# Kernel tuning notes

Measured on AMD Instinct MI355X. Metric: run time of the kernel, lower is better.

## Reference

```python
import jax, jax.numpy as jnp
import numpy as np

VOCAB, EMBED, HIDDEN = 50000, 300, 1024
BATCH, SEQ = 64, 128


def _lstm_params(key, in_dim, hid):
    k = 1.0 / np.sqrt(hid)
    k1, k2, k3, k4 = jax.random.split(key, 4)
    return (
        jax.random.uniform(k1, (4 * hid, in_dim), jnp.float32, -k, k),  # W_ih
        jax.random.uniform(k2, (4 * hid, hid), jnp.float32, -k, k),     # W_hh
        jax.random.uniform(k3, (4 * hid,), jnp.float32, -k, k),          # b_ih
        jax.random.uniform(k4, (4 * hid,), jnp.float32, -k, k),          # b_hh
    )


def setup_inputs() -> dict:
    key = jax.random.key(0)
    ke, kf, kb, ki = jax.random.split(key, 4)
    embed_table = jax.random.normal(ke, (VOCAB, EMBED), jnp.float32)
    Wih_f, Whh_f, bih_f, bhh_f = _lstm_params(kf, EMBED, HIDDEN)
    Wih_b, Whh_b, bih_b, bhh_b = _lstm_params(kb, EMBED, HIDDEN)
    inputs = jax.random.randint(ki, (BATCH, SEQ), 0, VOCAB, jnp.int64 if jax.config.jax_enable_x64 else jnp.int32)
    return {
        "embed_table": embed_table,
        "Wih_f": Wih_f, "Whh_f": Whh_f, "bih_f": bih_f, "bhh_f": bhh_f,
        "Wih_b": Wih_b, "Whh_b": Whh_b, "bih_b": bih_b, "bhh_b": bhh_b,
        "inputs": inputs,
    }


def _lstm_cell(x, h, c, Wih, Whh, bih, bhh):
    # torch.nn.LSTMCell gate layout: i, f, g, o
    gates = x @ Wih.T + h @ Whh.T + (bih + bhh)
    i, f, g, o = jnp.split(gates, 4, axis=-1)
    i, f, o = jax.nn.sigmoid(i), jax.nn.sigmoid(f), jax.nn.sigmoid(o)
    g = jnp.tanh(g)
    c_new = f * c + i * g
    h_new = o * jnp.tanh(c_new)
    return h_new, c_new


def reference(embed_table, Wih_f, Whh_f, bih_f, bhh_f, Wih_b, Whh_b, bih_b, bhh_b, inputs):
    embeds = embed_table[inputs]  # [B, T, E]
    B = inputs.shape[0]
    zeros = jnp.zeros((B, HIDDEN), embeds.dtype)
    # Faithful to the original bug: the forward loop always uses the all-zero
    # (never-updated) backward state and overwrites h each step, so the result
    # equals a single LSTMCell step on the LAST token with zero (h, c).
    h_fwd, _ = _lstm_cell(embeds[:, -1], zeros, zeros, Wih_f, Whh_f, bih_f, bhh_f)
    # Backward loop: h carries over, but c stays zero forever (bug preserved).
    xs = jnp.flip(embeds, axis=1).transpose(1, 0, 2)  # time-major, reversed: [T, B, E]

    def step(h, x):
        h_new, _ = _lstm_cell(x, h, zeros, Wih_b, Whh_b, bih_b, bhh_b)
        return h_new, None

    h_bwd, _ = jax.lax.scan(step, zeros, xs)
    return jnp.concatenate((h_fwd, h_bwd), axis=1)  # [B, 2*HIDDEN]
```

## Files before the change

### kernel.cpp

```cpp
#include <hip/hip_runtime.h>
#include <stdint.h>

static constexpr int BB = 64;
static constexpr int TT = 128;
static constexpr int EE = 300;
static constexpr int HH = 1024;
static constexpr int OUTW = 2 * HH;
static constexpr int NB  = 256;
static constexpr int NT  = 512;


typedef __attribute__((ext_vector_type(8))) short bf16x8;
typedef __attribute__((ext_vector_type(4))) float f32x4;
union U16 { uint4 u; bf16x8 v; };

__device__ __forceinline__ unsigned short f2bf(float f) {
  uint32_t u = __float_as_uint(f);
  uint32_t r = (u + 0x7fffu + ((u >> 16) & 1u)) >> 16;
  return (unsigned short)r;
}
__device__ __forceinline__ float bf2f(unsigned short h) {
  return __uint_as_float(((uint32_t)h) << 16);
}

__device__ __forceinline__ void gload16_sc(uint4& d, const void* p) {
  asm volatile("global_load_dwordx4 %0, %1, off sc0 sc1" : "=v"(d) : "v"(p));
}
__device__ __forceinline__ void gload16_nc(uint4& d, const void* p) {
  asm volatile("global_load_dwordx4 %0, %1, off" : "=v"(d) : "v"(p));
}

__global__ __launch_bounds__(256) void k_stage(const float* __restrict__ tbl,
                                               const int* __restrict__ inp,
                                               unsigned char* __restrict__ xfrag,
                                               float* __restrict__ xT0) {
  __shared__ float tile[EE * 65];
  __shared__ int toks[BB];
  const int s = blockIdx.x;
  const int tid = threadIdx.x;
  if (tid < BB) toks[tid] = inp[tid * TT + (TT - 1 - s)];
  __syncthreads();
  for (int f = tid; f < BB * EE; f += 256) {
    int b = f / EE, e = f - b * EE;
    tile[e * 65 + b] = tbl[(size_t)toks[b] * EE + e];
  }
  __syncthreads();
  if (s == 0) {
    for (int f = tid; f < EE * BB; f += 256) {
      int e = f >> 6, b = f & 63;
      xT0[f] = tile[e * 65 + b];
    }
  }
  const int ksub = tid & 3, col = (tid >> 2) & 63;
  unsigned char* base = xfrag + (size_t)s * 98304;
  for (int kb = 0; kb < 12; ++kb) {
    uint32_t hi[4], lo[4];
#pragma unroll
    for (int j2 = 0; j2 < 4; ++j2) {
      int e0 = kb * 32 + ksub * 8 + 2 * j2;
      float f0 = (e0     < EE) ? tile[e0 * 65 + col]      : 0.f;
      float f1 = (e0 + 1 < EE) ? tile[(e0 + 1) * 65 + col] : 0.f;
      unsigned short h0 = f2bf(f0), h1 = f2bf(f1);
      unsigned short l0 = f2bf(f0 - bf2f(h0)), l1 = f2bf(f1 - bf2f(h1));
      hi[j2] = (uint32_t)h0 | ((uint32_t)h1 << 16);
      lo[j2] = (uint32_t)l0 | ((uint32_t)l1 << 16);
    }
    unsigned char* p = base + kb * 8192 + col * 128 + ksub * 16;
    *(uint4*)p        = make_uint4(hi[0], hi[1], hi[2], hi[3]);
    *(uint4*)(p + 64) = make_uint4(lo[0], lo[1], lo[2], lo[3]);
  }
}

__global__ __launch_bounds__(256) void k_fwd(const float* __restrict__ Wih,
                                             const float* __restrict__ bih,
                                             const float* __restrict__ bhh,
                                             const float* __restrict__ xT,
                                             float* __restrict__ out) {
  const int g = blockIdx.x * 256 + threadIdx.x;
  const int j = g >> 6, b = g & 63;
  const float* wi = Wih + (size_t)j * EE;
  const float* wg = Wih + (size_t)(2 * HH + j) * EE;
  const float* wo = Wih + (size_t)(3 * HH + j) * EE;
  float si = 0.f, sg = 0.f, so = 0.f;
  for (int e = 0; e < EE; ++e) {
    float x = xT[e * 64 + b];
    si += x * wi[e];
    sg += x * wg[e];
    so += x * wo[e];
  }
  si += bih[j] + bhh[j];
  sg += bih[2 * HH + j] + bhh[2 * HH + j];
  so += bih[3 * HH + j] + bhh[3 * HH + j];
  float iv = 1.f / (1.f + expf(-si));
  float gv = tanhf(sg);
  float ov = 1.f / (1.f + expf(-so));
  out[b * OUTW + j] = ov * tanhf(iv * gv);
}

__global__ __launch_bounds__(NT, 2) void k_rec(const float* __restrict__ Whh,
                                               const float* __restrict__ Wih,
                                               const float* __restrict__ bih,
                                               const float* __restrict__ bhh,
                                               const unsigned char* __restrict__ xfrag,
                                               unsigned char* __restrict__ h0ex,
                                               unsigned char* __restrict__ h1ex,
                                               unsigned int* __restrict__ syncc,
                                               float* __restrict__ out) {
  __shared__ float red[4 * 4 * 16 * 16];
  __shared__ float bias_s[12];

  const int tid  = threadIdx.x;
  const int bk   = blockIdx.x;
  const int lane = tid & 63;
  const int wv   = tid >> 6;
  const int w2   = wv >> 1;
  const int nh   = wv & 1;
  const int l15  = lane & 15;
  const int l4   = lane >> 4;
  const int j0   = bk * 4;

  if (tid < 12) {
    int u = tid / 3, gi = tid % 3;
    int grow = j0 + u + (gi == 0 ? 0 : (gi == 1 ? 2 * HH : 3 * HH));
    bias_s[tid] = bih[grow] + bhh[grow];
  }

  bf16x8 Ah[11], Al[11];
  {
    const int row = l15;
    const bool rv = row < 12;
    const int u = rv ? row / 3 : 0, gi = rv ? row % 3 : 0;
    const int grow = j0 + u + (gi == 0 ? 0 : (gi == 1 ? 2 * HH : 3 * HH));
#pragma unroll
    for (int c = 0; c < 11; ++c) {
      const int kb = w2 + 4 * c;
      const int k0 = kb * 32 + l4 * 8;
      U16 ah, al;
#pragma unroll
      for (int j2 = 0; j2 < 4; ++j2) {
        float f0 = 0.f, f1 = 0.f;
        if (rv) {
          int k = k0 + 2 * j2;
          if (k < HH) {
            f0 = Whh[(size_t)grow * HH + k];
            f1 = Whh[(size_t)grow * HH + k + 1];
          } else {
            int e = k - HH;
            if (e     < EE) f0 = Wih[(size_t)grow * EE + e];
            if (e + 1 < EE) f1 = Wih[(size_t)grow * EE + e + 1];
          }
        }
        unsigned short h0 = f2bf(f0), h1 = f2bf(f1);
        unsigned short q0 = f2bf(f0 - bf2f(h0)), q1 = f2bf(f1 - bf2f(h1));
        ((uint32_t*)&ah.u)[j2] = (uint32_t)h0 | ((uint32_t)h1 << 16);
        ((uint32_t*)&al.u)[j2] = (uint32_t)q0 | ((uint32_t)q1 << 16);
      }
      Ah[c] = ah.v;
      Al[c] = al.v;
    }
  }
  __syncthreads();

  const uint32_t c0h = (uint32_t)((nh * 32 + l15) * 128 + l4 * 16);
  const uint32_t c0l = c0h + 64;
  const uint32_t c1h = c0h + 16 * 128;
  const uint32_t c1l = c1h + 64;

  for (int s = 0; s < TT; ++s) {
    const unsigned char* hb = (s & 1) ? h1ex : h0ex;
    unsigned char*       hn = (s & 1) ? h0ex : h1ex;
    const unsigned char* xb = xfrag + (size_t)s * 98304;
    const unsigned char* hbase = hb + w2 * 8192;
    const unsigned char* xbase = xb + w2 * 8192;

    uint4 pb[2][4];
    gload16_sc(pb[0][0], hbase + c0h);
    gload16_sc(pb[0][1], hbase + c0l);
    gload16_sc(pb[0][2], hbase + c1h);
    gload16_sc(pb[0][3], hbase + c1l);

    f32x4 acc0 = {0.f, 0.f, 0.f, 0.f};
    f32x4 acc1 = {0.f, 0.f, 0.f, 0.f};

#pragma unroll
    for (int c = 0; c < 11; ++c) {
      if (c < 10) {
        const int cn = c + 1;
        if (cn < 8) {
          const unsigned char* p = hbase + (size_t)cn * 32768;
          gload16_sc(pb[cn & 1][0], p + c0h);
          gload16_sc(pb[cn & 1][1], p + c0l);
          gload16_sc(pb[cn & 1][2], p + c1h);
          gload16_sc(pb[cn & 1][3], p + c1l);
        } else {
          const unsigned char* p = xbase + (size_t)(cn - 8) * 32768;
          gload16_nc(pb[cn & 1][0], p + c0h);
          gload16_nc(pb[cn & 1][1], p + c0l);
          gload16_nc(pb[cn & 1][2], p + c1h);
          gload16_nc(pb[cn & 1][3], p + c1l);
        }
        asm volatile("s_waitcnt vmcnt(4)" ::: "memory");
      } else {
        asm volatile("s_waitcnt vmcnt(0)" ::: "memory");
      }
      __builtin_amdgcn_sched_barrier(0);

      U16 t0, t1, t2, t3;
      t0.u = pb[c & 1][0]; t1.u = pb[c & 1][1];
      t2.u = pb[c & 1][2]; t3.u = pb[c & 1][3];
      acc0 = __builtin_amdgcn_mfma_f32_16x16x32_bf16(Ah[c], t0.v, acc0, 0, 0, 0);
      acc1 = __builtin_amdgcn_mfma_f32_16x16x32_bf16(Ah[c], t2.v, acc1, 0, 0, 0);
      acc0 = __builtin_amdgcn_mfma_f32_16x16x32_bf16(Al[c], t0.v, acc0, 0, 0, 0);
      acc1 = __builtin_amdgcn_mfma_f32_16x16x32_bf16(Al[c], t2.v, acc1, 0, 0, 0);
      acc0 = __builtin_amdgcn_mfma_f32_16x16x32_bf16(Ah[c], t1.v, acc0, 0, 0, 0);
      acc1 = __builtin_amdgcn_mfma_f32_16x16x32_bf16(Ah[c], t3.v, acc1, 0, 0, 0);
    }

#pragma unroll
    for (int r = 0; r < 4; ++r) {
      red[(((w2 * 4) + (nh * 2 + 0)) * 16 + (l4 * 4 + r)) * 16 + l15] = acc0[r];
      red[(((w2 * 4) + (nh * 2 + 1)) * 16 + (l4 * 4 + r)) * 16 + l15] = acc1[r];
    }
    __syncthreads();

    if (tid < 256) {
      const int u = tid >> 6, b = tid & 63;
      const int t = b >> 4, c16 = b & 15;
      float g3[3];
#pragma unroll
      for (int gi = 0; gi < 3; ++gi) {
        const int row = u * 3 + gi;
        float sum = bias_s[row];
#pragma unroll
        for (int ww = 0; ww < 4; ++ww)
          sum += red[((ww * 4 + t) * 16 + row) * 16 + c16];
        g3[gi] = sum;
      }
      float iv = 1.f / (1.f + expf(-g3[0]));
      float gv = tanhf(g3[1]);
      float ov = 1.f / (1.f + expf(-g3[2]));
      float hv = ov * tanhf(iv * gv);

      const int k = j0 + u;
      const int kb = k >> 5, ks = (k >> 3) & 3, jj = k & 7;
      unsigned char* dh = hn + kb * 8192 + b * 128 + ks * 16 + jj * 2;
      unsigned short hhv = f2bf(hv);
      unsigned short llv = f2bf(hv - bf2f(hhv));
      asm volatile("global_store_short %0, %1, off sc0 sc1"
                   :: "v"(dh), "v"((uint32_t)hhv) : "memory");
      asm volatile("global_store_short %0, %1, off sc0 sc1"
                   :: "v"(dh + 64), "v"((uint32_t)llv) : "memory");
      if (s == TT - 1) out[b * OUTW + HH + k] = hv;
    }

    asm volatile("s_waitcnt vmcnt(0)" ::: "memory");
    __syncthreads();
    if (tid == 0) {
      atomicAdd(syncc, 1u);
      const unsigned int tgt = (unsigned int)(NB * (s + 1));
      unsigned int cur;
      do {
        __builtin_amdgcn_s_sleep(1);
        asm volatile("global_load_dword %0, %1, off sc0 sc1\n\t"
                     "s_waitcnt vmcnt(0)"
                     : "=v"(cur) : "v"(syncc) : "memory");
      } while (cur < tgt);
    }
    __syncthreads();
  }
}

extern "C" void kernel_launch(void* const* d_in, const int* in_sizes, int n_in,
                              void* d_out, int out_size, void* d_ws, size_t ws_size,
                              hipStream_t stream) {
  const float* tbl   = (const float*)d_in[0];
  const float* Wih_f = (const float*)d_in[1];
  const float* bih_f = (const float*)d_in[3];
  const float* bhh_f = (const float*)d_in[4];
  const float* Wih_b = (const float*)d_in[5];
  const float* Whh_b = (const float*)d_in[6];
  const float* bih_b = (const float*)d_in[7];
  const float* bhh_b = (const float*)d_in[8];
  const int*   inp   = (const int*)d_in[9];
  float* out = (float*)d_out;

  char* ws = (char*)d_ws;
  unsigned int*  syncc = (unsigned int*)ws;
  unsigned char* h0ex  = (unsigned char*)(ws + 1024);
  unsigned char* h1ex  = h0ex + 262144;
  float*         xT0   = (float*)(h1ex + 262144);
  unsigned char* xfrag = (unsigned char*)(ws + 602112);

  hipMemsetAsync(d_ws, 0, 1024 + 262144, stream);

  k_stage<<<dim3(TT), dim3(256), 0, stream>>>(tbl, inp, xfrag, xT0);
  k_fwd<<<dim3(256), dim3(256), 0, stream>>>(Wih_f, bih_f, bhh_f, xT0, out);

  void* args[] = { (void*)&Whh_b, (void*)&Wih_b, (void*)&bih_b, (void*)&bhh_b,
                   (void*)&xfrag, (void*)&h0ex, (void*)&h1ex, (void*)&syncc, (void*)&out };
  hipLaunchCooperativeKernel((void*)k_rec, dim3(NB), dim3(NT), args, 0, stream);
}
```

Baseline: 2.761 ms.

## Replace atomic grid barrier with per-block flag array and deepen load prefetch

The grid-wide step barrier drops the single atomic counter. Each block now writes its generation number to its own slot, and one wavefront polls all 256 slots with vector loads and a wave-wide all-check. The goal is to remove atomic contention on one address in the latency-bound recurrent loop. Separately, the h/x fragment prefetch goes from double to quad buffering, with three chunks in flight and graded vmcnt waits. This costs more registers and risks lower occupancy under launch_bounds(512,2).

```diff
diff --git a/kernel.cpp b/kernel.cpp
--- a/kernel.cpp
+++ b/kernel.cpp
@@ -104,7 +104,7 @@
                                                const unsigned char* __restrict__ xfrag,
                                                unsigned char* __restrict__ h0ex,
                                                unsigned char* __restrict__ h1ex,
-                                               unsigned int* __restrict__ syncc,
+                                               unsigned int* __restrict__ arr,
                                                float* __restrict__ out) {
   __shared__ float red[4 * 4 * 16 * 16];
   __shared__ float bias_s[12];
@@ -166,6 +166,20 @@
   const uint32_t c1h = c0h + 16 * 128;
   const uint32_t c1l = c1h + 64;
 
+#define ISSUE_H(cn)                                               \
+  { const unsigned char* p_ = hbase + (size_t)(cn) * 32768;       \
+    gload16_sc(pb[(cn) & 3][0], p_ + c0h);                        \
+    gload16_sc(pb[(cn) & 3][1], p_ + c0l);                        \
+    gload16_sc(pb[(cn) & 3][2], p_ + c1h);                        \
+    gload16_sc(pb[(cn) & 3][3], p_ + c1l); }
+#define ISSUE_X(cn)                                               \
+  { const unsigned char* p_ = xbase + (size_t)((cn) - 8) * 32768; \
+    gload16_nc(pb[(cn) & 3][0], p_ + c0h);                        \
+    gload16_nc(pb[(cn) & 3][1], p_ + c0l);                        \
+    gload16_nc(pb[(cn) & 3][2], p_ + c1h);                        \
+    gload16_nc(pb[(cn) & 3][3], p_ + c1l); }
+#define ISSUE(cn) { if ((cn) < 8) ISSUE_H(cn) else ISSUE_X(cn) }
+
   for (int s = 0; s < TT; ++s) {
     const unsigned char* hb = (s & 1) ? h1ex : h0ex;
     unsigned char*       hn = (s & 1) ? h0ex : h1ex;
@@ -173,32 +187,20 @@
     const unsigned char* hbase = hb + w2 * 8192;
     const unsigned char* xbase = xb + w2 * 8192;
 
-    uint4 pb[2][4];
-    gload16_sc(pb[0][0], hbase + c0h);
-    gload16_sc(pb[0][1], hbase + c0l);
-    gload16_sc(pb[0][2], hbase + c1h);
-    gload16_sc(pb[0][3], hbase + c1l);
+    uint4 pb[4][4];
+    ISSUE(0); ISSUE(1); ISSUE(2);
 
     f32x4 acc0 = {0.f, 0.f, 0.f, 0.f};
     f32x4 acc1 = {0.f, 0.f, 0.f, 0.f};
 
 #pragma unroll
     for (int c = 0; c < 11; ++c) {
-      if (c < 10) {
-        const int cn = c + 1;
-        if (cn < 8) {
-          const unsigned char* p = hbase + (size_t)cn * 32768;
-          gload16_sc(pb[cn & 1][0], p + c0h);
-          gload16_sc(pb[cn & 1][1], p + c0l);
-          gload16_sc(pb[cn & 1][2], p + c1h);
-          gload16_sc(pb[cn & 1][3], p + c1l);
-        } else {
-          const unsigned char* p = xbase + (size_t)(cn - 8) * 32768;
-          gload16_nc(pb[cn & 1][0], p + c0h);
-          gload16_nc(pb[cn & 1][1], p + c0l);
-          gload16_nc(pb[cn & 1][2], p + c1h);
-          gload16_nc(pb[cn & 1][3], p + c1l);
-        }
+      if (c + 3 < 11) {
+        ISSUE(c + 3);
+        asm volatile("s_waitcnt vmcnt(12)" ::: "memory");
+      } else if (c == 8) {
+        asm volatile("s_waitcnt vmcnt(8)" ::: "memory");
+      } else if (c == 9) {
         asm volatile("s_waitcnt vmcnt(4)" ::: "memory");
       } else {
         asm volatile("s_waitcnt vmcnt(0)" ::: "memory");
@@ -206,8 +208,8 @@
       __builtin_amdgcn_sched_barrier(0);
 
       U16 t0, t1, t2, t3;
-      t0.u = pb[c & 1][0]; t1.u = pb[c & 1][1];
-      t2.u = pb[c & 1][2]; t3.u = pb[c & 1][3];
+      t0.u = pb[c & 3][0]; t1.u = pb[c & 3][1];
+      t2.u = pb[c & 3][2]; t3.u = pb[c & 3][3];
       acc0 = __builtin_amdgcn_mfma_f32_16x16x32_bf16(Ah[c], t0.v, acc0, 0, 0, 0);
       acc1 = __builtin_amdgcn_mfma_f32_16x16x32_bf16(Ah[c], t2.v, acc1, 0, 0, 0);
       acc0 = __builtin_amdgcn_mfma_f32_16x16x32_bf16(Al[c], t0.v, acc0, 0, 0, 0);
@@ -255,19 +257,30 @@
 
     asm volatile("s_waitcnt vmcnt(0)" ::: "memory");
     __syncthreads();
-    if (tid == 0) {
-      atomicAdd(syncc, 1u);
-      const unsigned int tgt = (unsigned int)(NB * (s + 1));
-      unsigned int cur;
-      do {
+    if (wv == 0) {
+      const uint32_t gen = (uint32_t)(s + 1);
+      if (lane == 0) {
+        unsigned int* slot = arr + bk;
+        asm volatile("global_store_dword %0, %1, off sc0 sc1"
+                     :: "v"(slot), "v"(gen) : "memory");
+      }
+      asm volatile("s_waitcnt vmcnt(0)" ::: "memory");
+      const unsigned int* pl = arr + lane * 4;
+      for (;;) {
+        uint4 a;
+        asm volatile("global_load_dwordx4 %0, %1, off sc0 sc1\n\t"
+                     "s_waitcnt vmcnt(0)"
+                     : "=v"(a) : "v"(pl) : "memory");
+        int ok = (a.x >= gen) && (a.y >= gen) && (a.z >= gen) && (a.w >= gen);
+        if (__all(ok)) break;
         __builtin_amdgcn_s_sleep(1);
-        asm volatile("global_load_dword %0, %1, off sc0 sc1\n\t"
-                     "s_waitcnt vmcnt(0)"
-                     : "=v"(cur) : "v"(syncc) : "memory");
-      } while (cur < tgt);
+      }
     }
     __syncthreads();
   }
+#undef ISSUE
+#undef ISSUE_H
+#undef ISSUE_X
 }
 
 extern "C" void kernel_launch(void* const* d_in, const int* in_sizes, int n_in,
@@ -285,7 +298,7 @@
   float* out = (float*)d_out;
 
   char* ws = (char*)d_ws;
-  unsigned int*  syncc = (unsigned int*)ws;
+  unsigned int*  arr   = (unsigned int*)ws;
   unsigned char* h0ex  = (unsigned char*)(ws + 1024);
   unsigned char* h1ex  = h0ex + 262144;
   float*         xT0   = (float*)(h1ex + 262144);
@@ -297,6 +310,6 @@
   k_fwd<<<dim3(256), dim3(256), 0, stream>>>(Wih_f, bih_f, bhh_f, xT0, out);
 
   void* args[] = { (void*)&Whh_b, (void*)&Wih_b, (void*)&bih_b, (void*)&bhh_b,
-                   (void*)&xfrag, (void*)&h0ex, (void*)&h1ex, (void*)&syncc, (void*)&out };
+                   (void*)&xfrag, (void*)&h0ex, (void*)&h1ex, (void*)&arr, (void*)&out };
   hipLaunchCooperativeKernel((void*)k_rec, dim3(NB), dim3(NT), args, 0, stream);
 }
```

Measured after the change: 2.243 ms. -18.8%, faster.
